# Performance work log

Hardware: AMD Instinct MI355X
Metric: run time of the kernel (lower is better)

The kernel has to match this reference:

```python
import jax, jax.numpy as jnp
import numpy as np

B = 16384
NUM_INPUTS = 256
ACTION_DIM = 16
H0 = 1024
H1 = 1024
K = 128  # num_support
MIN_BIN_WIDTH = 0.001
MIN_BIN_HEIGHT = 0.001
MIN_DERIVATIVE = 0.001
EDGE_CONST = float(np.log(np.exp(1.0 - 0.001) - 1.0))  # log(exp(0.999)-1)
LN_EPS = 1e-5


def setup_inputs() -> dict:
    key = jax.random.key(0)
    ks = jax.random.split(key, 16)
    def lin(kw, kb, fan_out, fan_in):
        w = 1.0 / np.sqrt(fan_in)
        W = jax.random.uniform(kw, (fan_out, fan_in), jnp.float32, -w, w)
        b = jax.random.uniform(kb, (fan_out,), jnp.float32, -w, w)
        return W, b
    w1, b1 = lin(ks[0], ks[1], H0, NUM_INPUTS)
    w2, b2 = lin(ks[2], ks[3], H1, H0 + ACTION_DIM)
    wv, bv = lin(ks[4], ks[5], 3 * K - 1, H1)
    wa = jax.random.uniform(ks[6], (1, H1), jnp.float32, -0.003, 0.003)
    ba = jax.random.uniform(ks[7], (1,), jnp.float32, -0.0003, 0.0003)
    wb = jax.random.uniform(ks[8], (1, H1), jnp.float32, -0.003, 0.003)
    bb = jax.random.uniform(ks[9], (1,), jnp.float32, -0.0003, 0.0003)
    return {
        "inputs": jax.random.normal(ks[10], (B, NUM_INPUTS), jnp.float32),
        "actions": jax.random.normal(ks[11], (B, ACTION_DIM), jnp.float32),
        "w1": w1, "b1": b1,
        "ln1_g": jnp.ones((H0,), jnp.float32), "ln1_b": jnp.zeros((H0,), jnp.float32),
        "w2": w2, "b2": b2,
        "ln2_g": jnp.ones((H1,), jnp.float32), "ln2_b": jnp.zeros((H1,), jnp.float32),
        "wv": wv, "bv": bv,
        "wa": wa, "ba": ba,
        "wb": wb, "bb": bb,
    }


def _layernorm(x, g, b):
    mu = jnp.mean(x, axis=-1, keepdims=True)
    var = jnp.mean((x - mu) ** 2, axis=-1, keepdims=True)
    return (x - mu) / jnp.sqrt(var + LN_EPS) * g + b


def reference(inputs, actions, w1, b1, ln1_g, ln1_b, w2, b2, ln2_g, ln2_b,
              wv, bv, wa, ba, wb, bb):
    # trunk MLP
    x = jax.nn.relu(_layernorm(inputs @ w1.T + b1, ln1_g, ln1_b))
    x = jnp.concatenate([x, actions], axis=1)
    x = jax.nn.relu(_layernorm(x @ w2.T + b2, ln2_g, ln2_b))

    spline_param = x @ wv.T + bv            # [B, 3K-1]
    scale_a = jnp.exp(x @ wa.T + ba)        # [B, 1]
    scale_b = x @ wb.T + bb                 # [B, 1]

    W = spline_param[:, :K]
    H = spline_param[:, K:2 * K]
    Draw = spline_param[:, 2 * K:]          # [B, K-1]

    W = MIN_BIN_WIDTH + (1 - MIN_BIN_WIDTH * K) * jax.nn.softmax(W, axis=1)
    H = MIN_BIN_HEIGHT + (1 - MIN_BIN_HEIGHT * K) * jax.nn.softmax(H, axis=1)
    Dmid = MIN_DERIVATIVE + jax.nn.softplus(Draw)
    edge = jnp.full((W.shape[0], 1), EDGE_CONST, W.dtype)
    D = jnp.concatenate([edge, Dmid, edge], axis=-1)  # [B, K+1]

    zeros = jnp.zeros((W.shape[0], 1), W.dtype)
    cumwidths = jnp.concatenate([zeros, jnp.cumsum(W, axis=-1)], axis=-1)
    cumwidths = cumwidths.at[..., -1].set(1.0)        # [B, K+1]
    widths = cumwidths[..., 1:] - cumwidths[..., :-1]

    cumheights = jnp.concatenate([zeros, jnp.cumsum(H, axis=-1)], axis=-1)
    cumheights = scale_a * cumheights + scale_b       # [B, K+1]
    heights = cumheights[..., 1:] - cumheights[..., :-1]

    tau = (jnp.arange(K, dtype=W.dtype) + 0.5) / K    # [K]

    # brute-force searchsorted: sum(tau >= cumwidths) - 1
    bin_idx = jnp.sum(tau[None, :, None] >= cumwidths[:, None, :], axis=-1) - 1  # [B,K]

    gather = lambda t: jnp.take_along_axis(t, bin_idx, axis=-1)
    input_cumwidths = gather(cumwidths)
    input_bin_widths = gather(widths)
    input_cumheights = gather(cumheights)
    input_heights = gather(heights)
    delta = heights / widths
    input_delta = gather(delta)
    input_derivatives = gather(D)
    input_derivatives_plus_one = gather(D[..., 1:])

    theta = (tau[None, :] - input_cumwidths) / input_bin_widths
    theta_one_minus = theta * (1 - theta)
    numerator = input_heights * (input_delta * theta ** 2 + input_derivatives * theta_one_minus)
    denominator = input_delta + (input_derivatives + input_derivatives_plus_one - 2 * input_delta) * theta_one_minus
    return input_cumheights + numerator / denominator  # [B, K]
```

## Files before the change

kernel.cpp:

```cpp
#include <hip/hip_runtime.h>
#include <hip/hip_bf16.h>
#include <math.h>

#define BROWS      16384
#define LN_EPS_F   1e-5f
#define MINW       0.001f
#define MINH       0.001f
#define MIND       0.001f
#define EDGE_CONST_F 0.5397423505783211f

typedef __bf16 bf16x8 __attribute__((ext_vector_type(8)));
typedef float  f32x4  __attribute__((ext_vector_type(4)));

__device__ __forceinline__ ushort f2bf(float x) {
    union { float f; unsigned u; } v; v.f = x;
    unsigned u = v.u;
    u += 0x7fffu + ((u >> 16) & 1u);
    return (ushort)(u >> 16);
}
__device__ __forceinline__ float bf2f(ushort h) {
    union { unsigned u; float f; } v; v.u = ((unsigned)h) << 16;
    return v.f;
}

__global__ __launch_bounds__(256, 2)
void gemm_bf16x3(const ushort* __restrict__ Ah, const ushort* __restrict__ Al,
                 const ushort* __restrict__ Bh, const ushort* __restrict__ Bl,
                 const float* __restrict__ bias,
                 float* __restrict__ C, int ldc, int Nstore, int Kpad)
{
    __shared__ ushort lds[32768];
    const int tid  = threadIdx.x;
    const int wid  = tid >> 6;
    const int lane = tid & 63;
    const int bm0  = blockIdx.x * 128;
    const int bn0  = blockIdx.y * 128;
    const int wm   = wid >> 1;
    const int wn   = wid & 1;
    const int l15  = lane & 15;
    const int kg   = lane >> 4;

    const ushort* gsrc[8];
    {
        const ushort* pb[4] = {Ah, Al, Bh, Bl};
        #pragma unroll
        for (int i = 0; i < 8; ++i) {
            const int F     = i * 4096 + tid * 16;
            const int pl    = F >> 13;
            const int chunk = (F & 8191) >> 4;
            const int kgrp  = chunk >> 7;
            const int row   = chunk & 127;
            const int r0    = (pl < 2) ? bm0 : bn0;
            gsrc[i] = pb[pl] + (size_t)(r0 + row) * Kpad + kgrp * 8;
        }
    }
    #define STAGE(bufbase, kelem)                                              \
        _Pragma("unroll")                                                      \
        for (int i = 0; i < 8; ++i) {                                          \
            __builtin_amdgcn_global_load_lds(                                  \
                (const __attribute__((address_space(1))) void*)(gsrc[i] + (kelem)), \
                (__attribute__((address_space(3))) void*)(&lds[(bufbase) + i * 2048 + wid * 512]), \
                16, 0, 0);                                                     \
        }

    f32x4 acc[4][4];
    #pragma unroll
    for (int m = 0; m < 4; ++m)
        #pragma unroll
        for (int n = 0; n < 4; ++n)
            acc[m][n] = (f32x4){0.f, 0.f, 0.f, 0.f};

    const int aoff = kg * 1024 + (wm * 64 + l15) * 8;
    const int boff = 8192 + kg * 1024 + (wn * 64 + l15) * 8;
    const int nt = Kpad >> 5;

    STAGE(0, 0);
    int cur = 0;

    for (int t = 0; t < nt; ++t) {
        const int nxt = cur ^ 1;
        if (t + 1 < nt) {
            STAGE(nxt * 16384, (t + 1) * 32);
            asm volatile("s_waitcnt vmcnt(8)" ::: "memory");
        } else {
            asm volatile("s_waitcnt vmcnt(0)" ::: "memory");
        }
        __builtin_amdgcn_sched_barrier(0);
        __builtin_amdgcn_s_barrier();
        asm volatile("" ::: "memory");

        const int cb = cur * 16384;
        bf16x8 aH[4], aL[4], bH[4], bL[4];
        #pragma unroll
        for (int m = 0; m < 4; ++m) {
            aH[m] = *(const bf16x8*)&lds[cb + aoff + m * 128];
            aL[m] = *(const bf16x8*)&lds[cb + 4096 + aoff + m * 128];
        }
        #pragma unroll
        for (int n = 0; n < 4; ++n) {
            bH[n] = *(const bf16x8*)&lds[cb + boff + n * 128];
            bL[n] = *(const bf16x8*)&lds[cb + 4096 + boff + n * 128];
        }

        __builtin_amdgcn_s_setprio(1);
        #pragma unroll
        for (int m = 0; m < 4; ++m)
            #pragma unroll
            for (int n = 0; n < 4; ++n)
                acc[m][n] = __builtin_amdgcn_mfma_f32_16x16x32_bf16(aH[m], bH[n], acc[m][n], 0, 0, 0);
        #pragma unroll
        for (int m = 0; m < 4; ++m)
            #pragma unroll
            for (int n = 0; n < 4; ++n)
                acc[m][n] = __builtin_amdgcn_mfma_f32_16x16x32_bf16(aH[m], bL[n], acc[m][n], 0, 0, 0);
        #pragma unroll
        for (int m = 0; m < 4; ++m)
            #pragma unroll
            for (int n = 0; n < 4; ++n)
                acc[m][n] = __builtin_amdgcn_mfma_f32_16x16x32_bf16(aL[m], bH[n], acc[m][n], 0, 0, 0);
        __builtin_amdgcn_s_setprio(0);

        asm volatile("s_waitcnt lgkmcnt(0)" ::: "memory");
        __builtin_amdgcn_sched_barrier(0);
        __builtin_amdgcn_s_barrier();
        asm volatile("" ::: "memory");
        cur = nxt;
    }
    #undef STAGE

    #pragma unroll
    for (int n = 0; n < 4; ++n) {
        const int col = bn0 + wn * 64 + n * 16 + l15;
        if (col < Nstore) {
            const float bs = bias[col];
            #pragma unroll
            for (int m = 0; m < 4; ++m) {
                const int row = bm0 + wm * 64 + m * 16 + kg * 4;
                #pragma unroll
                for (int r = 0; r < 4; ++r)
                    C[(size_t)(row + r) * ldc + col] = acc[m][n][r] + bs;
            }
        }
    }
}

__global__ __launch_bounds__(256)
void ln_relu_split(const float* __restrict__ Y,
                   const float* __restrict__ g, const float* __restrict__ b,
                   ushort* __restrict__ Xh, ushort* __restrict__ Xl, int xstride,
                   const float* __restrict__ actions, int dopad)
{
    __shared__ float red[4];
    const int row = blockIdx.x;
    const int tid = threadIdx.x;
    const float* y = Y + (size_t)row * 1024;

    const float4 v = *(const float4*)(y + tid * 4);
    float s = v.x + v.y + v.z + v.w;
    #pragma unroll
    for (int off = 32; off > 0; off >>= 1) s += __shfl_down(s, off, 64);
    if ((tid & 63) == 0) red[tid >> 6] = s;
    __syncthreads();
    const float mu = (red[0] + red[1] + red[2] + red[3]) * (1.f / 1024.f);
    __syncthreads();
    const float d0 = v.x - mu, d1 = v.y - mu, d2 = v.z - mu, d3 = v.w - mu;
    float s2 = d0 * d0 + d1 * d1 + d2 * d2 + d3 * d3;
    #pragma unroll
    for (int off = 32; off > 0; off >>= 1) s2 += __shfl_down(s2, off, 64);
    if ((tid & 63) == 0) red[tid >> 6] = s2;
    __syncthreads();
    const float var = (red[0] + red[1] + red[2] + red[3]) * (1.f / 1024.f);
    const float inv = 1.0f / sqrtf(var + LN_EPS_F);

    float o0 = fmaxf(0.f, d0 * inv * g[tid * 4 + 0] + b[tid * 4 + 0]);
    float o1 = fmaxf(0.f, d1 * inv * g[tid * 4 + 1] + b[tid * 4 + 1]);
    float o2 = fmaxf(0.f, d2 * inv * g[tid * 4 + 2] + b[tid * 4 + 2]);
    float o3 = fmaxf(0.f, d3 * inv * g[tid * 4 + 3] + b[tid * 4 + 3]);

    ushort4 oh, ol;
    oh.x = f2bf(o0); ol.x = f2bf(o0 - bf2f(oh.x));
    oh.y = f2bf(o1); ol.y = f2bf(o1 - bf2f(oh.y));
    oh.z = f2bf(o2); ol.z = f2bf(o2 - bf2f(oh.z));
    oh.w = f2bf(o3); ol.w = f2bf(o3 - bf2f(oh.w));
    *(ushort4*)(Xh + (size_t)row * xstride + tid * 4) = oh;
    *(ushort4*)(Xl + (size_t)row * xstride + tid * 4) = ol;

    if (actions != nullptr && tid < 16) {
        const float a = actions[(size_t)row * 16 + tid];
        const ushort h = f2bf(a);
        Xh[(size_t)row * xstride + 1024 + tid] = h;
        Xl[(size_t)row * xstride + 1024 + tid] = f2bf(a - bf2f(h));
    }
    if (dopad && tid >= 16 && tid < 64) {
        Xh[(size_t)row * xstride + 1024 + tid] = 0;
        Xl[(size_t)row * xstride + 1024 + tid] = 0;
    }
}

__global__ __launch_bounds__(256)
void split_mat(const float* __restrict__ src, int scols,
               ushort* __restrict__ Dh, ushort* __restrict__ Dl,
               int dcols, int total)
{
    const int idx = (blockIdx.x * 256 + threadIdx.x) * 4;
    if (idx >= total) return;
    const int r = idx / dcols, c = idx % dcols;
    float e[4];
    if (c + 3 < scols) {
        const float4 v = *(const float4*)(src + (size_t)r * scols + c);
        e[0] = v.x; e[1] = v.y; e[2] = v.z; e[3] = v.w;
    } else {
        #pragma unroll
        for (int j = 0; j < 4; ++j)
            e[j] = (c + j < scols) ? src[(size_t)r * scols + c + j] : 0.f;
    }
    ushort4 h, l;
    h.x = f2bf(e[0]); l.x = f2bf(e[0] - bf2f(h.x));
    h.y = f2bf(e[1]); l.y = f2bf(e[1] - bf2f(h.y));
    h.z = f2bf(e[2]); l.z = f2bf(e[2] - bf2f(h.z));
    h.w = f2bf(e[3]); l.w = f2bf(e[3] - bf2f(h.w));
    *(ushort4*)(Dh + idx) = h;
    *(ushort4*)(Dl + idx) = l;
}

__global__ __launch_bounds__(256)
void build_wcat_split(const float* __restrict__ wv, const float* __restrict__ wa,
                      const float* __restrict__ wb, const float* __restrict__ bv,
                      const float* __restrict__ ba, const float* __restrict__ bb,
                      ushort* __restrict__ Wh, ushort* __restrict__ Wl,
                      float* __restrict__ bcat)
{
    const int idx = blockIdx.x * 256 + threadIdx.x;
    if (idx < 512 * 1024) {
        const int n = idx >> 10, k = idx & 1023;
        const float v = (n < 383) ? wv[n * 1024 + k]
                       : (n == 383) ? wa[k]
                       : (n == 384) ? wb[k] : 0.f;
        const ushort h = f2bf(v);
        Wh[idx] = h;
        Wl[idx] = f2bf(v - bf2f(h));
    }
    if (idx < 512) {
        bcat[idx] = (idx < 383) ? bv[idx] : (idx == 383) ? ba[0]
                   : (idx == 384) ? bb[0] : 0.f;
    }
}

__device__ __forceinline__ float softplus_f(float x) {
    return (x > 20.f) ? x : log1pf(expf(x));
}

__global__ __launch_bounds__(256)
void spline_rq(const float* __restrict__ P, float* __restrict__ Out)
{
    __shared__ float cw[4][132];
    __shared__ float ch[4][132];
    __shared__ float Dv[4][132];
    const int wid  = threadIdx.x >> 6;
    const int lane = threadIdx.x & 63;
    const int r    = blockIdx.x * 4 + wid;
    const float* p = P + (size_t)r * 385;
    const int e0 = 2 * lane, e1 = 2 * lane + 1;

    const float sa = expf(p[383]);
    const float sb = p[384];

    const float w0 = p[e0], w1 = p[e1];
    float mx = fmaxf(w0, w1);
    #pragma unroll
    for (int off = 1; off < 64; off <<= 1) mx = fmaxf(mx, __shfl_xor(mx, off, 64));
    const float xw0 = expf(w0 - mx), xw1 = expf(w1 - mx);
    float sw = xw0 + xw1;
    #pragma unroll
    for (int off = 1; off < 64; off <<= 1) sw += __shfl_xor(sw, off, 64);
    const float cwn = (1.f - MINW * 128.f) / sw;
    const float Wv0 = MINW + cwn * xw0;
    const float Wv1 = MINW + cwn * xw1;
    float s = Wv0 + Wv1;
    #pragma unroll
    for (int off = 1; off < 64; off <<= 1) {
        const float t = __shfl_up(s, off, 64);
        if (lane >= off) s += t;
    }
    if (lane == 0) cw[wid][0] = 0.f;
    cw[wid][e1]     = s - Wv1;
    cw[wid][e1 + 1] = (lane == 63) ? 1.0f : s;

    const float h0 = p[128 + e0], h1 = p[128 + e1];
    float mh = fmaxf(h0, h1);
    #pragma unroll
    for (int off = 1; off < 64; off <<= 1) mh = fmaxf(mh, __shfl_xor(mh, off, 64));
    const float xh0 = expf(h0 - mh), xh1 = expf(h1 - mh);
    float sh = xh0 + xh1;
    #pragma unroll
    for (int off = 1; off < 64; off <<= 1) sh += __shfl_xor(sh, off, 64);
    const float chn = (1.f - MINH * 128.f) / sh;
    const float Hv0 = MINH + chn * xh0;
    const float Hv1 = MINH + chn * xh1;
    float t2 = Hv0 + Hv1;
    #pragma unroll
    for (int off = 1; off < 64; off <<= 1) {
        const float t = __shfl_up(t2, off, 64);
        if (lane >= off) t2 += t;
    }
    if (lane == 0) ch[wid][0] = sb;
    ch[wid][e1]     = sa * (t2 - Hv1) + sb;
    ch[wid][e1 + 1] = sa * t2 + sb;

    if (lane == 0) { Dv[wid][0] = EDGE_CONST_F; Dv[wid][128] = EDGE_CONST_F; }
    Dv[wid][e0 + 1] = MIND + softplus_f(p[256 + e0]);
    if (lane < 63) Dv[wid][e1 + 1] = MIND + softplus_f(p[256 + e1]);

    __syncthreads();

    #pragma unroll
    for (int t = 0; t < 2; ++t) {
        const int e = 2 * lane + t;
        const float tau = ((float)e + 0.5f) * (1.f / 128.f);
        int lo = 0, hi = 128;
        #pragma unroll
        for (int it = 0; it < 7; ++it) {
            const int mid = (lo + hi) >> 1;
            if (cw[wid][mid] <= tau) lo = mid; else hi = mid;
        }
        const int bin = lo;
        const float icw = cw[wid][bin];
        const float ibw = cw[wid][bin + 1] - icw;
        const float ich = ch[wid][bin];
        const float ih  = ch[wid][bin + 1] - ich;
        const float idelta = ih / ibw;
        const float dd0 = Dv[wid][bin];
        const float dd1 = Dv[wid][bin + 1];
        const float theta = (tau - icw) / ibw;
        const float tom = theta * (1.f - theta);
        const float num = ih * (idelta * theta * theta + dd0 * tom);
        const float den = idelta + (dd0 + dd1 - 2.f * idelta) * tom;
        Out[(size_t)r * 128 + e] = ich + num / den;
    }
}

extern "C" void kernel_launch(void* const* d_in, const int* in_sizes, int n_in,
                              void* d_out, int out_size, void* d_ws, size_t ws_size,
                              hipStream_t stream) {
    const float* inputs  = (const float*)d_in[0];
    const float* actions = (const float*)d_in[1];
    const float* w1      = (const float*)d_in[2];
    const float* b1      = (const float*)d_in[3];
    const float* ln1_g   = (const float*)d_in[4];
    const float* ln1_b   = (const float*)d_in[5];
    const float* w2      = (const float*)d_in[6];
    const float* b2      = (const float*)d_in[7];
    const float* ln2_g   = (const float*)d_in[8];
    const float* ln2_b   = (const float*)d_in[9];
    const float* wv      = (const float*)d_in[10];
    const float* bv      = (const float*)d_in[11];
    const float* wa      = (const float*)d_in[12];
    const float* ba      = (const float*)d_in[13];
    const float* wb      = (const float*)d_in[14];
    const float* bb      = (const float*)d_in[15];

    float*  ws_y  = (float*)d_ws;
    ushort* ws_Xh = (ushort*)(ws_y + (size_t)16384 * 1024);
    ushort* ws_Xl = ws_Xh + (size_t)16384 * 1088;
    ushort* w1h   = ws_Xl + (size_t)16384 * 1088;
    ushort* w1l   = w1h + 1024 * 256;
    ushort* w2h   = w1l + 1024 * 256;
    ushort* w2l   = w2h + 1024 * 1088;
    ushort* wch   = w2l + 1024 * 1088;
    ushort* wcl   = wch + 512 * 1024;
    float*  bcat  = (float*)(wcl + 512 * 1024);

    split_mat<<<(16384 * 256 / 4 + 255) / 256, 256, 0, stream>>>(inputs, 256, ws_Xh, ws_Xl, 256, 16384 * 256);
    split_mat<<<(1024 * 256 / 4 + 255) / 256, 256, 0, stream>>>(w1, 256, w1h, w1l, 256, 1024 * 256);
    split_mat<<<(1024 * 1088 / 4 + 255) / 256, 256, 0, stream>>>(w2, 1040, w2h, w2l, 1088, 1024 * 1088);
    build_wcat_split<<<(512 * 1024 + 255) / 256, 256, 0, stream>>>(wv, wa, wb, bv, ba, bb, wch, wcl, bcat);

    gemm_bf16x3<<<dim3(128, 8), 256, 0, stream>>>(ws_Xh, ws_Xl, w1h, w1l, b1, ws_y, 1024, 1024, 256);
    ln_relu_split<<<16384, 256, 0, stream>>>(ws_y, ln1_g, ln1_b, ws_Xh, ws_Xl, 1088, actions, 1);

    gemm_bf16x3<<<dim3(128, 8), 256, 0, stream>>>(ws_Xh, ws_Xl, w2h, w2l, b2, ws_y, 1024, 1024, 1088);
    ln_relu_split<<<16384, 256, 0, stream>>>(ws_y, ln2_g, ln2_b, ws_Xh, ws_Xl, 1024, nullptr, 0);

    gemm_bf16x3<<<dim3(128, 4), 256, 0, stream>>>(ws_Xh, ws_Xl, wch, wcl, bcat, ws_y, 385, 385, 1024);

    spline_rq<<<4096, 256, 0, stream>>>(ws_y, (float*)d_out);
}
```

Baseline: 432.6 us.

## Interleave global-to-LDS prefetch loads across the three MFMA phases

The eight async global-to-LDS prefetch loads for the next K tile are split into groups issued between the three MFMA passes (hi*hi, hi*lo, lo*hi). LDS fragment reads are likewise split so each pass only loads the operands it needs. Each phase gets its own lgkmcnt wait and barrier. The goal is to spread memory traffic across the compute and shorten register live ranges, at the cost of two extra workgroup barriers per iteration.

```diff
diff --git a/kernel.cpp b/kernel.cpp
--- a/kernel.cpp
+++ b/kernel.cpp
@@ -54,14 +54,11 @@
             gsrc[i] = pb[pl] + (size_t)(r0 + row) * Kpad + kgrp * 8;
         }
     }
-    #define STAGE(bufbase, kelem)                                              \
-        _Pragma("unroll")                                                      \
-        for (int i = 0; i < 8; ++i) {                                          \
-            __builtin_amdgcn_global_load_lds(                                  \
-                (const __attribute__((address_space(1))) void*)(gsrc[i] + (kelem)), \
-                (__attribute__((address_space(3))) void*)(&lds[(bufbase) + i * 2048 + wid * 512]), \
-                16, 0, 0);                                                     \
-        }
+    #define STAGE_ONE(i, bufbase, kelem)                                       \
+        __builtin_amdgcn_global_load_lds(                                      \
+            (const __attribute__((address_space(1))) void*)(gsrc[i] + (kelem)),\
+            (__attribute__((address_space(3))) void*)(&lds[(bufbase) + (i) * 2048 + wid * 512]), \
+            16, 0, 0)
 
     f32x4 acc[4][4];
     #pragma unroll
@@ -74,59 +71,73 @@
     const int boff = 8192 + kg * 1024 + (wn * 64 + l15) * 8;
     const int nt = Kpad >> 5;
 
-    STAGE(0, 0);
+    STAGE_ONE(0, 0, 0); STAGE_ONE(1, 0, 0); STAGE_ONE(2, 0, 0); STAGE_ONE(3, 0, 0);
+    STAGE_ONE(4, 0, 0); STAGE_ONE(5, 0, 0); STAGE_ONE(6, 0, 0); STAGE_ONE(7, 0, 0);
     int cur = 0;
 
     for (int t = 0; t < nt; ++t) {
         const int nxt = cur ^ 1;
-        if (t + 1 < nt) {
-            STAGE(nxt * 16384, (t + 1) * 32);
-            asm volatile("s_waitcnt vmcnt(8)" ::: "memory");
-        } else {
-            asm volatile("s_waitcnt vmcnt(0)" ::: "memory");
-        }
+        const int nb  = nxt * 16384;
+        const int cb  = cur * 16384;
+        const int ke  = (t + 1) * 32;
+        const bool pf = (t + 1 < nt);
+
+        if (pf) { STAGE_ONE(0, nb, ke); STAGE_ONE(1, nb, ke); STAGE_ONE(2, nb, ke); }
+        if (pf) { asm volatile("s_waitcnt vmcnt(3)" ::: "memory"); }
+        else    { asm volatile("s_waitcnt vmcnt(0)" ::: "memory"); }
         __builtin_amdgcn_sched_barrier(0);
         __builtin_amdgcn_s_barrier();
         asm volatile("" ::: "memory");
 
-        const int cb = cur * 16384;
         bf16x8 aH[4], aL[4], bH[4], bL[4];
         #pragma unroll
-        for (int m = 0; m < 4; ++m) {
-            aH[m] = *(const bf16x8*)&lds[cb + aoff + m * 128];
-            aL[m] = *(const bf16x8*)&lds[cb + 4096 + aoff + m * 128];
-        }
-        #pragma unroll
-        for (int n = 0; n < 4; ++n) {
-            bH[n] = *(const bf16x8*)&lds[cb + boff + n * 128];
-            bL[n] = *(const bf16x8*)&lds[cb + 4096 + boff + n * 128];
-        }
-
+        for (int m = 0; m < 4; ++m) aH[m] = *(const bf16x8*)&lds[cb + aoff + m * 128];
+        #pragma unroll
+        for (int n = 0; n < 4; ++n) bH[n] = *(const bf16x8*)&lds[cb + boff + n * 128];
+        asm volatile("s_waitcnt lgkmcnt(0)" ::: "memory");
+        __builtin_amdgcn_sched_barrier(0);
         __builtin_amdgcn_s_setprio(1);
         #pragma unroll
         for (int m = 0; m < 4; ++m)
             #pragma unroll
             for (int n = 0; n < 4; ++n)
                 acc[m][n] = __builtin_amdgcn_mfma_f32_16x16x32_bf16(aH[m], bH[n], acc[m][n], 0, 0, 0);
+        __builtin_amdgcn_s_setprio(0);
+        __builtin_amdgcn_s_barrier();
+        asm volatile("" ::: "memory");
+
+        if (pf) { STAGE_ONE(3, nb, ke); STAGE_ONE(4, nb, ke); STAGE_ONE(5, nb, ke); }
+        #pragma unroll
+        for (int n = 0; n < 4; ++n) bL[n] = *(const bf16x8*)&lds[cb + 4096 + boff + n * 128];
+        asm volatile("s_waitcnt lgkmcnt(0)" ::: "memory");
+        __builtin_amdgcn_sched_barrier(0);
+        __builtin_amdgcn_s_setprio(1);
         #pragma unroll
         for (int m = 0; m < 4; ++m)
             #pragma unroll
             for (int n = 0; n < 4; ++n)
                 acc[m][n] = __builtin_amdgcn_mfma_f32_16x16x32_bf16(aH[m], bL[n], acc[m][n], 0, 0, 0);
+        __builtin_amdgcn_s_setprio(0);
+        __builtin_amdgcn_s_barrier();
+        asm volatile("" ::: "memory");
+
+        if (pf) { STAGE_ONE(6, nb, ke); STAGE_ONE(7, nb, ke); }
+        #pragma unroll
+        for (int m = 0; m < 4; ++m) aL[m] = *(const bf16x8*)&lds[cb + 4096 + aoff + m * 128];
+        asm volatile("s_waitcnt lgkmcnt(0)" ::: "memory");
+        __builtin_amdgcn_sched_barrier(0);
+        __builtin_amdgcn_s_setprio(1);
         #pragma unroll
         for (int m = 0; m < 4; ++m)
             #pragma unroll
             for (int n = 0; n < 4; ++n)
                 acc[m][n] = __builtin_amdgcn_mfma_f32_16x16x32_bf16(aL[m], bH[n], acc[m][n], 0, 0, 0);
         __builtin_amdgcn_s_setprio(0);
-
-        asm volatile("s_waitcnt lgkmcnt(0)" ::: "memory");
-        __builtin_amdgcn_sched_barrier(0);
         __builtin_amdgcn_s_barrier();
         asm volatile("" ::: "memory");
         cur = nxt;
     }
-    #undef STAGE
+    #undef STAGE_ONE
 
     #pragma unroll
     for (int n = 0; n < 4; ++n) {
```

New measurement: 433.1 us. No clear change (+0.1%).

## Single-buffer swizzled LDS GEMM with higher occupancy and reduced K padding

Applied to the files above, without the earlier changes.

Replaces the double-buffered bf16x3 GEMM with a single-buffered version that uses half the LDS. That allows three blocks per CU, and an XOR swizzle on the LDS layout reduces bank conflicts. Low-part fragments are loaded lazily to lower register pressure. The K padding for the second layer drops from 1088 to 1056 to cut wasted MFMA work. The cost is that prefetch overlap is lost, so each tile now waits on its global loads before computing, relying on other resident blocks to hide that latency.

```diff
diff --git a/kernel.cpp b/kernel.cpp
--- a/kernel.cpp
+++ b/kernel.cpp
@@ -23,45 +23,41 @@
     return v.f;
 }
 
-__global__ __launch_bounds__(256, 2)
-void gemm_bf16x3(const ushort* __restrict__ Ah, const ushort* __restrict__ Al,
-                 const ushort* __restrict__ Bh, const ushort* __restrict__ Bl,
-                 const float* __restrict__ bias,
-                 float* __restrict__ C, int ldc, int Nstore, int Kpad)
-{
-    __shared__ ushort lds[32768];
+template<int DUMMY>
+__global__ __launch_bounds__(256, 3)
+void gemm_bf16x3_sb(const ushort* __restrict__ Ah, const ushort* __restrict__ Al,
+                    const ushort* __restrict__ Bh, const ushort* __restrict__ Bl,
+                    const float* __restrict__ bias,
+                    float* __restrict__ C, int ldc, int Nstore, int Kpad)
+{
+    __shared__ ushort lds[16384];
+    constexpr int AH0 = 0, AL0 = 4096, BH0 = 8192, BL0 = 12288;
+
     const int tid  = threadIdx.x;
     const int wid  = tid >> 6;
     const int lane = tid & 63;
-    const int bm0  = blockIdx.x * 128;
-    const int bn0  = blockIdx.y * 128;
     const int wm   = wid >> 1;
     const int wn   = wid & 1;
     const int l15  = lane & 15;
     const int kg   = lane >> 4;
-
-    const ushort* gsrc[8];
+    const int bm0  = blockIdx.x * 128;
+    const int bn0  = blockIdx.y * 128;
+
+    const ushort* sP[8];
     {
         const ushort* pb[4] = {Ah, Al, Bh, Bl};
         #pragma unroll
-        for (int i = 0; i < 8; ++i) {
-            const int F     = i * 4096 + tid * 16;
-            const int pl    = F >> 13;
-            const int chunk = (F & 8191) >> 4;
-            const int kgrp  = chunk >> 7;
-            const int row   = chunk & 127;
-            const int r0    = (pl < 2) ? bm0 : bn0;
-            gsrc[i] = pb[pl] + (size_t)(r0 + row) * Kpad + kgrp * 8;
-        }
-    }
-    #define STAGE(bufbase, kelem)                                              \
-        _Pragma("unroll")                                                      \
-        for (int i = 0; i < 8; ++i) {                                          \
-            __builtin_amdgcn_global_load_lds(                                  \
-                (const __attribute__((address_space(1))) void*)(gsrc[i] + (kelem)), \
-                (__attribute__((address_space(3))) void*)(&lds[(bufbase) + i * 2048 + wid * 512]), \
-                16, 0, 0);                                                     \
-        }
+        for (int j = 0; j < 8; ++j) {
+            const int pl  = j >> 1;
+            const int c   = (j & 1) * 256 + tid;
+            const int pr  = c >> 3;
+            const int s   = (c & 7) ^ (pr & 7);
+            const int row = pr * 2 + (s >> 2);
+            const int kgv = s & 3;
+            const int r0  = (pl < 2) ? bm0 : bn0;
+            sP[j] = pb[pl] + (size_t)(r0 + row) * Kpad + kgv * 8;
+        }
+    }
 
     f32x4 acc[4][4];
     #pragma unroll
@@ -70,63 +66,59 @@
         for (int n = 0; n < 4; ++n)
             acc[m][n] = (f32x4){0.f, 0.f, 0.f, 0.f};
 
-    const int aoff = kg * 1024 + (wm * 64 + l15) * 8;
-    const int boff = 8192 + kg * 1024 + (wn * 64 + l15) * 8;
+    const int slotA = (((lane & 1) * 4 + kg) ^ (l15 >> 1)) * 8;
+    const int aswz  = wm * 2048 + (l15 >> 1) * 64 + slotA;
+    const int bswz  = wn * 2048 + (l15 >> 1) * 64 + slotA;
     const int nt = Kpad >> 5;
 
-    STAGE(0, 0);
-    int cur = 0;
-
     for (int t = 0; t < nt; ++t) {
-        const int nxt = cur ^ 1;
-        if (t + 1 < nt) {
-            STAGE(nxt * 16384, (t + 1) * 32);
-            asm volatile("s_waitcnt vmcnt(8)" ::: "memory");
-        } else {
-            asm volatile("s_waitcnt vmcnt(0)" ::: "memory");
-        }
-        __builtin_amdgcn_sched_barrier(0);
-        __builtin_amdgcn_s_barrier();
-        asm volatile("" ::: "memory");
-
-        const int cb = cur * 16384;
-        bf16x8 aH[4], aL[4], bH[4], bL[4];
-        #pragma unroll
-        for (int m = 0; m < 4; ++m) {
-            aH[m] = *(const bf16x8*)&lds[cb + aoff + m * 128];
-            aL[m] = *(const bf16x8*)&lds[cb + 4096 + aoff + m * 128];
-        }
-        #pragma unroll
-        for (int n = 0; n < 4; ++n) {
-            bH[n] = *(const bf16x8*)&lds[cb + boff + n * 128];
-            bL[n] = *(const bf16x8*)&lds[cb + 4096 + boff + n * 128];
-        }
-
+        const int ke = t * 32;
+        #pragma unroll
+        for (int j = 0; j < 8; ++j)
+            __builtin_amdgcn_global_load_lds(
+                (const __attribute__((address_space(1))) void*)(sP[j] + ke),
+                (__attribute__((address_space(3))) void*)(&lds[j * 2048 + wid * 512]),
+                16, 0, 0);
+        __syncthreads();
+
+        bf16x8 aH[4], bH[4];
+        #pragma unroll
+        for (int m = 0; m < 4; ++m) aH[m] = *(const bf16x8*)&lds[AH0 + aswz + m * 512];
+        #pragma unroll
+        for (int n = 0; n < 4; ++n) bH[n] = *(const bf16x8*)&lds[BH0 + bswz + n * 512];
         __builtin_amdgcn_s_setprio(1);
         #pragma unroll
         for (int m = 0; m < 4; ++m)
             #pragma unroll
             for (int n = 0; n < 4; ++n)
                 acc[m][n] = __builtin_amdgcn_mfma_f32_16x16x32_bf16(aH[m], bH[n], acc[m][n], 0, 0, 0);
-        #pragma unroll
-        for (int m = 0; m < 4; ++m)
-            #pragma unroll
-            for (int n = 0; n < 4; ++n)
-                acc[m][n] = __builtin_amdgcn_mfma_f32_16x16x32_bf16(aH[m], bL[n], acc[m][n], 0, 0, 0);
-        #pragma unroll
-        for (int m = 0; m < 4; ++m)
-            #pragma unroll
-            for (int n = 0; n < 4; ++n)
-                acc[m][n] = __builtin_amdgcn_mfma_f32_16x16x32_bf16(aL[m], bH[n], acc[m][n], 0, 0, 0);
         __builtin_amdgcn_s_setprio(0);
-
-        asm volatile("s_waitcnt lgkmcnt(0)" ::: "memory");
-        __builtin_amdgcn_sched_barrier(0);
-        __builtin_amdgcn_s_barrier();
-        asm volatile("" ::: "memory");
-        cur = nxt;
-    }
-    #undef STAGE
+        {
+            bf16x8 aL[4];
+            #pragma unroll
+            for (int m = 0; m < 4; ++m) aL[m] = *(const bf16x8*)&lds[AL0 + aswz + m * 512];
+            __builtin_amdgcn_s_setprio(1);
+            #pragma unroll
+            for (int m = 0; m < 4; ++m)
+                #pragma unroll
+                for (int n = 0; n < 4; ++n)
+                    acc[m][n] = __builtin_amdgcn_mfma_f32_16x16x32_bf16(aL[m], bH[n], acc[m][n], 0, 0, 0);
+            __builtin_amdgcn_s_setprio(0);
+        }
+        {
+            bf16x8 bL[4];
+            #pragma unroll
+            for (int n = 0; n < 4; ++n) bL[n] = *(const bf16x8*)&lds[BL0 + bswz + n * 512];
+            __builtin_amdgcn_s_setprio(1);
+            #pragma unroll
+            for (int m = 0; m < 4; ++m)
+                #pragma unroll
+                for (int n = 0; n < 4; ++n)
+                    acc[m][n] = __builtin_amdgcn_mfma_f32_16x16x32_bf16(aH[m], bL[n], acc[m][n], 0, 0, 0);
+            __builtin_amdgcn_s_setprio(0);
+        }
+        __syncthreads();
+    }
 
     #pragma unroll
     for (int n = 0; n < 4; ++n) {
@@ -191,7 +183,7 @@
         Xh[(size_t)row * xstride + 1024 + tid] = h;
         Xl[(size_t)row * xstride + 1024 + tid] = f2bf(a - bf2f(h));
     }
-    if (dopad && tid >= 16 && tid < 64) {
+    if (dopad && tid >= 16 && tid < 32) {
         Xh[(size_t)row * xstride + 1024 + tid] = 0;
         Xl[(size_t)row * xstride + 1024 + tid] = 0;
     }
@@ -361,27 +353,27 @@
 
     float*  ws_y  = (float*)d_ws;
     ushort* ws_Xh = (ushort*)(ws_y + (size_t)16384 * 1024);
-    ushort* ws_Xl = ws_Xh + (size_t)16384 * 1088;
-    ushort* w1h   = ws_Xl + (size_t)16384 * 1088;
+    ushort* ws_Xl = ws_Xh + (size_t)16384 * 1056;
+    ushort* w1h   = ws_Xl + (size_t)16384 * 1056;
     ushort* w1l   = w1h + 1024 * 256;
     ushort* w2h   = w1l + 1024 * 256;
-    ushort* w2l   = w2h + 1024 * 1088;
-    ushort* wch   = w2l + 1024 * 1088;
+    ushort* w2l   = w2h + 1024 * 1056;
+    ushort* wch   = w2l + 1024 * 1056;
     ushort* wcl   = wch + 512 * 1024;
     float*  bcat  = (float*)(wcl + 512 * 1024);
 
     split_mat<<<(16384 * 256 / 4 + 255) / 256, 256, 0, stream>>>(inputs, 256, ws_Xh, ws_Xl, 256, 16384 * 256);
     split_mat<<<(1024 * 256 / 4 + 255) / 256, 256, 0, stream>>>(w1, 256, w1h, w1l, 256, 1024 * 256);
-    split_mat<<<(1024 * 1088 / 4 + 255) / 256, 256, 0, stream>>>(w2, 1040, w2h, w2l, 1088, 1024 * 1088);
+    split_mat<<<(1024 * 1056 / 4 + 255) / 256, 256, 0, stream>>>(w2, 1040, w2h, w2l, 1056, 1024 * 1056);
     build_wcat_split<<<(512 * 1024 + 255) / 256, 256, 0, stream>>>(wv, wa, wb, bv, ba, bb, wch, wcl, bcat);
 
-    gemm_bf16x3<<<dim3(128, 8), 256, 0, stream>>>(ws_Xh, ws_Xl, w1h, w1l, b1, ws_y, 1024, 1024, 256);
-    ln_relu_split<<<16384, 256, 0, stream>>>(ws_y, ln1_g, ln1_b, ws_Xh, ws_Xl, 1088, actions, 1);
-
-    gemm_bf16x3<<<dim3(128, 8), 256, 0, stream>>>(ws_Xh, ws_Xl, w2h, w2l, b2, ws_y, 1024, 1024, 1088);
+    gemm_bf16x3_sb<0><<<dim3(128, 8), 256, 0, stream>>>(ws_Xh, ws_Xl, w1h, w1l, b1, ws_y, 1024, 1024, 256);
+    ln_relu_split<<<16384, 256, 0, stream>>>(ws_y, ln1_g, ln1_b, ws_Xh, ws_Xl, 1056, actions, 1);
+
+    gemm_bf16x3_sb<0><<<dim3(128, 8), 256, 0, stream>>>(ws_Xh, ws_Xl, w2h, w2l, b2, ws_y, 1024, 1024, 1056);
     ln_relu_split<<<16384, 256, 0, stream>>>(ws_y, ln2_g, ln2_b, ws_Xh, ws_Xl, 1024, nullptr, 0);
 
-    gemm_bf16x3<<<dim3(128, 4), 256, 0, stream>>>(ws_Xh, ws_Xl, wch, wcl, bcat, ws_y, 385, 385, 1024);
+    gemm_bf16x3_sb<0><<<dim3(128, 4), 256, 0, stream>>>(ws_Xh, ws_Xl, wch, wcl, bcat, ws_y, 385, 385, 1024);
 
     spline_rq<<<4096, 256, 0, stream>>>(ws_y, (float*)d_out);
 }
```

New measurement: 372.5 us. 13.9% less time.
